# Optimization experiments

Hardware: AMD Instinct MI355X
Metric: run time of the kernel (lower is better)

The kernel has to match this reference:

```python
import jax, jax.numpy as jnp
import numpy as np
import math

H = 16          # num_heads
BS = 512        # block_size


def setup_inputs() -> dict:
    key = jax.random.key(0)
    ks = jax.random.split(key, 5)
    B, S, D = 2, 8192, 1024
    return {
        "x": jax.random.normal(ks[0], (B, S, D), dtype=jnp.float32),
        "W_qkv": jax.random.normal(ks[1], (D, 3 * D), dtype=jnp.float32) * (1.0 / math.sqrt(D)),
        "b_qkv": jax.random.normal(ks[2], (3 * D,), dtype=jnp.float32) * 0.02,
        "W_out": jax.random.normal(ks[3], (D, D), dtype=jnp.float32) * (1.0 / math.sqrt(D)),
        "b_out": jax.random.normal(ks[4], (D,), dtype=jnp.float32) * 0.02,
    }


def reference(x, W_qkv, b_qkv, W_out, b_out):
    B, S, D = x.shape
    hd = D // H
    nb = S // BS  # S chosen divisible by block_size, so no padding branch
    scale = 1.0 / math.sqrt(hd)

    qkv = (x @ W_qkv + b_qkv).reshape(B, S, 3, H, hd)
    qkv = jnp.transpose(qkv, (2, 0, 3, 1, 4))  # [3, B, H, S, hd]
    q, k, v = qkv[0], qkv[1], qkv[2]

    # split into blocks: [B, H, nb, BS, hd]
    qb = q.reshape(B, H, nb, BS, hd)
    kb = k.reshape(B, H, nb, BS, hd)
    vb = v.reshape(B, H, nb, BS, hd)

    # local block attention (separate softmax, as in original)
    s1 = jnp.einsum('bhnid,bhnjd->bhnij', qb, kb) * scale
    o1 = jnp.einsum('bhnij,bhnjd->bhnid', jax.nn.softmax(s1, axis=-1), vb)

    # next-block (ring) attention with its own softmax, then summed
    kn = jnp.roll(kb, -1, axis=2)
    vn = jnp.roll(vb, -1, axis=2)
    s2 = jnp.einsum('bhnid,bhnjd->bhnij', qb, kn) * scale
    o2 = jnp.einsum('bhnij,bhnjd->bhnid', jax.nn.softmax(s2, axis=-1), vn)

    out = (o1 + o2).reshape(B, H, S, hd)            # [B, H, S, hd]
    out = jnp.transpose(out, (0, 2, 1, 3)).reshape(B, S, D)
    return out @ W_out + b_out
```

## Files before the change

kernel.cpp:

```cpp
#include <hip/hip_runtime.h>
#include <hip/hip_bf16.h>

typedef __attribute__((ext_vector_type(4))) float f32x4;
typedef __attribute__((ext_vector_type(8))) short s16x8;
typedef __attribute__((address_space(3))) unsigned int lds_uint;
typedef __attribute__((address_space(1))) const unsigned int g_uint;

static __device__ __forceinline__ unsigned short f2b(float f) {
    union { __hip_bfloat16 h; unsigned short u; } c;
    c.h = __float2bfloat16(f);
    return c.u;
}

static __device__ __forceinline__ void async_copy16(const void* gsrc, void* ldst) {
    __builtin_amdgcn_global_load_lds((g_uint*)gsrc, (lds_uint*)ldst, 16, 0, 0);
}

__global__ __launch_bounds__(256) void cvt_x_kernel(const float* __restrict__ x,
                                                    unsigned short* __restrict__ xb) {
    long i = ((long)blockIdx.x * 256 + threadIdx.x) * 8;
    float4 a = *(const float4*)(x + i);
    float4 b = *(const float4*)(x + i + 4);
    union { unsigned short s[8]; s16x8 v; } o;
    o.s[0] = f2b(a.x); o.s[1] = f2b(a.y); o.s[2] = f2b(a.z); o.s[3] = f2b(a.w);
    o.s[4] = f2b(b.x); o.s[5] = f2b(b.y); o.s[6] = f2b(b.z); o.s[7] = f2b(b.w);
    *(s16x8*)(xb + i) = o.v;
}

__global__ __launch_bounds__(256) void cvt_wT_kernel(const float* __restrict__ W,
                                                     unsigned short* __restrict__ Wt,
                                                     int K, int N) {
    __shared__ float T[64][65];
    int nbk = K >> 6;
    int bk = blockIdx.x % nbk;
    int bn = blockIdx.x / nbk;
    int t = threadIdx.x;
    int r = t >> 4, c4 = (t & 15) << 2;
#pragma unroll
    for (int rd = 0; rd < 4; ++rd) {
        int row = rd * 16 + r;
        float4 v = *(const float4*)(W + (long)(bk * 64 + row) * N + bn * 64 + c4);
        T[row][c4 + 0] = v.x; T[row][c4 + 1] = v.y;
        T[row][c4 + 2] = v.z; T[row][c4 + 3] = v.w;
    }
    __syncthreads();
#pragma unroll
    for (int rd = 0; rd < 4; ++rd) {
        int nrow = rd * 16 + r;
        union { unsigned short s[4]; unsigned long long u; } o;
#pragma unroll
        for (int j = 0; j < 4; ++j) o.s[j] = f2b(T[c4 + j][nrow]);
        *(unsigned long long*)(Wt + (long)(bn * 64 + nrow) * K + bk * 64 + c4) = o.u;
    }
}

template<int OM>
__global__ __launch_bounds__(512) void gemm256_kernel(const unsigned short* __restrict__ A,
                                                      const unsigned short* __restrict__ Bt,
                                                      const float* __restrict__ bias,
                                                      unsigned short* __restrict__ qkb,
                                                      unsigned short* __restrict__ vT,
                                                      float* __restrict__ Cf,
                                                      int ntileN) {
    __shared__ char lds[131072];
    const int tid = threadIdx.x;
    const int w = tid >> 6, wm = w >> 2, wn = w & 3;
    const int l = tid & 63, c = l & 15, g = l >> 4;
    const int cpx = gridDim.x >> 3;
    const int wg = (blockIdx.x & 7) * cpx + (blockIdx.x >> 3);
    const int tm = wg / ntileN, tn = wg % ntileN;
    const long m0 = (long)tm << 8, n0 = (long)tn << 8;
    const int swg = (g ^ ((c >> 1) & 3)) << 4;
    const int ssch = (tid & 3) ^ ((tid >> 3) & 3);
    const int rb = tid >> 2;

    f32x4 acc[8][4];
#pragma unroll
    for (int i = 0; i < 8; ++i)
#pragma unroll
        for (int j = 0; j < 4; ++j) acc[i][j] = (f32x4){0.f, 0.f, 0.f, 0.f};

#define STG(panel, p0, u, kh, isB) do { \
    char* blk_ = lds + ((isB) ? 65536 : 0) + (((((u) & 1) * 2 + (kh))) << 14); \
    const unsigned short* sp_ = (panel) + (u) * 64 + (kh) * 32 + ssch * 8; \
    async_copy16(sp_ + ((p0) + rb) * 1024L, blk_ + tid * 16); \
    async_copy16(sp_ + ((p0) + 128 + rb) * 1024L, blk_ + 8192 + tid * 16); \
} while (0)

    STG(Bt, n0, 0, 0, 1); STG(A, m0, 0, 0, 0); STG(Bt, n0, 0, 1, 1); STG(A, m0, 0, 1, 0);
    STG(Bt, n0, 1, 0, 1); STG(A, m0, 1, 0, 0); STG(Bt, n0, 1, 1, 1);
    asm volatile("s_waitcnt vmcnt(10)");
    __builtin_amdgcn_s_barrier();
    __builtin_amdgcn_sched_barrier(0);

#define PHASE_MFMA(IBASE) \
    __builtin_amdgcn_s_setprio(1); \
    _Pragma("unroll") for (int i_ = 0; i_ < 4; ++i_) \
    _Pragma("unroll") for (int j_ = 0; j_ < 4; ++j_) \
        acc[(IBASE) + i_][j_] = __builtin_amdgcn_mfma_f32_16x16x32_bf16(af[i_], bf[j_], acc[(IBASE) + i_][j_], 0, 0, 0); \
    __builtin_amdgcn_s_setprio(0);

#define GSTEP(s, ST1, ST2, ST3, ST4, VMID, VEND) do { \
    const int buf_ = (s) & 1; \
    const char* LA0 = lds + ((buf_ * 2 + 0) << 14); \
    const char* LA1 = lds + ((buf_ * 2 + 1) << 14); \
    const char* LB0 = lds + 65536 + ((buf_ * 2 + 0) << 14); \
    const char* LB1 = lds + 65536 + ((buf_ * 2 + 1) << 14); \
    s16x8 af[4], bf[4]; \
    _Pragma("unroll") for (int i = 0; i < 4; ++i) af[i] = *(const s16x8*)(LA0 + (wm * 128 + i * 16 + c) * 64 + swg); \
    _Pragma("unroll") for (int j = 0; j < 4; ++j) bf[j] = *(const s16x8*)(LB0 + (wn * 64 + j * 16 + c) * 64 + swg); \
    if (ST1) STG(A, m0, (s) + 1, 1, 0); \
    __builtin_amdgcn_s_barrier(); \
    PHASE_MFMA(0) \
    __builtin_amdgcn_s_barrier(); \
    __builtin_amdgcn_sched_barrier(0); \
    _Pragma("unroll") for (int i = 0; i < 4; ++i) af[i] = *(const s16x8*)(LA0 + (wm * 128 + (4 + i) * 16 + c) * 64 + swg); \
    if (ST2) STG(Bt, n0, (s) + 2, 0, 1); \
    __builtin_amdgcn_s_barrier(); \
    PHASE_MFMA(4) \
    asm volatile("s_waitcnt " VMID); \
    __builtin_amdgcn_s_barrier(); \
    __builtin_amdgcn_sched_barrier(0); \
    _Pragma("unroll") for (int i = 0; i < 4; ++i) af[i] = *(const s16x8*)(LA1 + (wm * 128 + i * 16 + c) * 64 + swg); \
    _Pragma("unroll") for (int j = 0; j < 4; ++j) bf[j] = *(const s16x8*)(LB1 + (wn * 64 + j * 16 + c) * 64 + swg); \
    if (ST3) STG(A, m0, (s) + 2, 0, 0); \
    __builtin_amdgcn_s_barrier(); \
    PHASE_MFMA(0) \
    __builtin_amdgcn_s_barrier(); \
    __builtin_amdgcn_sched_barrier(0); \
    _Pragma("unroll") for (int i = 0; i < 4; ++i) af[i] = *(const s16x8*)(LA1 + (wm * 128 + (4 + i) * 16 + c) * 64 + swg); \
    if (ST4) STG(Bt, n0, (s) + 2, 1, 1); \
    __builtin_amdgcn_s_barrier(); \
    PHASE_MFMA(4) \
    if (VEND) { asm volatile("s_waitcnt " VMID##_E); } \
    __builtin_amdgcn_s_barrier(); \
    __builtin_amdgcn_sched_barrier(0); \
} while (0)

#define VM10 "vmcnt(10)"
#define VM10_E "vmcnt(10)"
#define VM8 "vmcnt(8)"
#define VM8_E "vmcnt(4)"
#define VM0 "vmcnt(0)"
#define VM0_E "vmcnt(0)"

    for (int s = 0; s < 14; ++s) GSTEP(s, 1, 1, 1, 1, VM10, 1);
    GSTEP(14, 1, 0, 0, 0, VM8, 1);
    GSTEP(15, 0, 0, 0, 0, VM0, 0);

    const long mrow0 = m0 + wm * 128;
    const int ncol0 = (int)n0 + wn * 64;
    if (OM == 0) {
        if (ncol0 < 2048) {
#pragma unroll
            for (int j = 0; j < 4; ++j) {
                int n = ncol0 + j * 16 + c;
                float bv = bias[n];
#pragma unroll
                for (int i = 0; i < 8; ++i)
#pragma unroll
                    for (int r = 0; r < 4; ++r) {
                        long m = mrow0 + i * 16 + 4 * g + r;
                        qkb[m * 2048 + n] = f2b(acc[i][j][r] + bv);
                    }
            }
        } else {
#pragma unroll
            for (int j = 0; j < 4; ++j) {
                int n = ncol0 + j * 16 + c;
                float bv = bias[n];
                int h = (n - 2048) >> 6, hd = n & 63;
#pragma unroll
                for (int i = 0; i < 8; ++i) {
                    long m = mrow0 + i * 16 + 4 * g;
                    long bb = m >> 13, ss = m & 8191;
                    union { unsigned short sh[4]; unsigned long long u; } o;
#pragma unroll
                    for (int r = 0; r < 4; ++r) o.sh[r] = f2b(acc[i][j][r] + bv);
                    *(unsigned long long*)(vT + ((bb * 16 + h) * 64 + hd) * 8192 + ss) = o.u;
                }
            }
        }
    } else {
#pragma unroll
        for (int j = 0; j < 4; ++j) {
            int n = ncol0 + j * 16 + c;
            float bv = bias[n];
#pragma unroll
            for (int i = 0; i < 8; ++i)
#pragma unroll
                for (int r = 0; r < 4; ++r) {
                    long m = mrow0 + i * 16 + 4 * g + r;
                    Cf[m * 1024 + n] = acc[i][j][r] + bv;
                }
        }
    }
#undef STG
#undef PHASE_MFMA
#undef GSTEP
}

__global__ __launch_bounds__(256) void attn_kernel(const unsigned short* __restrict__ qkb,
                                                   const unsigned short* __restrict__ vT,
                                                   unsigned short* __restrict__ outp) {
    __shared__ __align__(16) char KV[4][8192];
    __shared__ unsigned short Pws[4][32 * 72];
    const int bid = blockIdx.x;
    const int wgid = (bid & 7) * 256 + (bid >> 3);
    const int qt = wgid & 3;
    const int nblk = (wgid >> 2) & 15;
    const int h = (wgid >> 6) & 15;
    const int b = wgid >> 10;
    const int tid = threadIdx.x;
    const int w = tid >> 6, l = tid & 63;
    const int c = l & 15, g = l >> 4;

    const long qrow0 = (long)b * 8192 + nblk * 512 + qt * 128 + w * 32 + c;
    s16x8 qf[2][2];
#pragma unroll
    for (int qg = 0; qg < 2; ++qg) {
        const unsigned short* qp = qkb + (qrow0 + qg * 16) * 2048 + h * 64;
        qf[qg][0] = *(const s16x8*)(qp + g * 8);
        qf[qg][1] = *(const s16x8*)(qp + 32 + g * 8);
    }

    char* pw = (char*)(&Pws[w][0]);
    const float C2 = 0.125f * 1.44269504088896f;

    const int cl = tid & 7, rw = tid >> 3;
    const int sc = cl ^ (rw & 7);
    const int kb1 = (nblk + 1) & 15;
    const unsigned short* Kg0 = qkb + ((long)b * 8192 + nblk * 512 + rw) * 2048 + 1024 + h * 64 + sc * 8;
    const unsigned short* Kg1 = qkb + ((long)b * 8192 + kb1 * 512 + rw) * 2048 + 1024 + h * 64 + sc * 8;
    const unsigned short* Vg0 = vT + ((long)(b * 16 + h) * 64 + rw) * 8192 + nblk * 512 + sc * 8;
    const unsigned short* Vg1 = vT + ((long)(b * 16 + h) * 64 + rw) * 8192 + kb1 * 512 + sc * 8;

#define STAGE(tile) do { \
    const unsigned short* kn_ = (((tile) & 8) ? Kg1 : Kg0) + ((long)((tile) & 7) << 17); \
    const unsigned short* vn_ = (((tile) & 8) ? Vg1 : Vg0) + (((tile) & 7) << 6); \
    char* kd_ = KV[(tile) & 1] + tid * 16; \
    char* vd_ = KV[2 + ((tile) & 1)] + tid * 16; \
    async_copy16(kn_, kd_); \
    async_copy16(kn_ + 32L * 2048, kd_ + 4096); \
    async_copy16(vn_, vd_); \
    async_copy16(vn_ + 32L * 8192, vd_ + 4096); \
} while (0)

    float outv[2][16];
#pragma unroll
    for (int qg = 0; qg < 2; ++qg)
#pragma unroll
        for (int i = 0; i < 16; ++i) outv[qg][i] = 0.f;
    f32x4 oac[2][4];
#pragma unroll
    for (int qg = 0; qg < 2; ++qg)
#pragma unroll
        for (int i = 0; i < 4; ++i) oac[qg][i] = (f32x4){0.f, 0.f, 0.f, 0.f};
    float mrun[2] = {-3e38f, -3e38f}, lrun[2] = {0.f, 0.f};

    const int ch0 = (g ^ (c & 7)) << 4;

    STAGE(0);

    for (int it = 0; it < 16; ++it) {
        if (it < 15) {
            STAGE(it + 1);
            asm volatile("s_waitcnt vmcnt(4)" ::: "memory");
        } else {
            asm volatile("s_waitcnt vmcnt(0)" ::: "memory");
        }
        __builtin_amdgcn_s_barrier();
        __builtin_amdgcn_sched_barrier(0);

        const char* Kc = KV[it & 1];
        const char* Vc = KV[2 + (it & 1)];

        f32x4 sac[2][4];
#pragma unroll
        for (int qg = 0; qg < 2; ++qg)
#pragma unroll
            for (int i = 0; i < 4; ++i) sac[qg][i] = (f32x4){0.f, 0.f, 0.f, 0.f};
        __builtin_amdgcn_s_setprio(1);
#pragma unroll
        for (int kt = 0; kt < 4; ++kt) {
            const char* kr = Kc + (kt * 16 + c) * 128;
            s16x8 a0 = *(const s16x8*)(kr + ch0);
            s16x8 a1 = *(const s16x8*)(kr + (ch0 ^ 64));
            sac[0][kt] = __builtin_amdgcn_mfma_f32_16x16x32_bf16(a0, qf[0][0], sac[0][kt], 0, 0, 0);
            sac[0][kt] = __builtin_amdgcn_mfma_f32_16x16x32_bf16(a1, qf[0][1], sac[0][kt], 0, 0, 0);
            sac[1][kt] = __builtin_amdgcn_mfma_f32_16x16x32_bf16(a0, qf[1][0], sac[1][kt], 0, 0, 0);
            sac[1][kt] = __builtin_amdgcn_mfma_f32_16x16x32_bf16(a1, qf[1][1], sac[1][kt], 0, 0, 0);
        }
        __builtin_amdgcn_s_setprio(0);

#pragma unroll
        for (int qg = 0; qg < 2; ++qg) {
            float mx = sac[qg][0][0];
#pragma unroll
            for (int kt = 0; kt < 4; ++kt)
#pragma unroll
                for (int r = 0; r < 4; ++r) mx = fmaxf(mx, sac[qg][kt][r]);
            mx = fmaxf(mx, __shfl_xor(mx, 16, 64));
            mx = fmaxf(mx, __shfl_xor(mx, 32, 64));
            float mnew = fmaxf(mrun[qg], mx);
            float alpha = exp2f((mrun[qg] - mnew) * C2);
            float ls = 0.f;
#pragma unroll
            for (int kt = 0; kt < 4; ++kt) {
                union { unsigned short sh[4]; unsigned long long u; } pk;
#pragma unroll
                for (int r = 0; r < 4; ++r) {
                    float e = exp2f((sac[qg][kt][r] - mnew) * C2);
                    ls += e;
                    pk.sh[r] = f2b(e);
                }
                *(unsigned long long*)(pw + (qg * 16 + c) * 144 + kt * 32 + g * 8) = pk.u;
            }
            lrun[qg] = lrun[qg] * alpha + ls;
            mrun[qg] = mnew;
#pragma unroll
            for (int i = 0; i < 4; ++i) oac[qg][i] *= alpha;
        }

        __builtin_amdgcn_s_setprio(1);
#pragma unroll
        for (int kf = 0; kf < 2; ++kf) {
            s16x8 pf0 = *(const s16x8*)(pw + c * 144 + kf * 64 + g * 16);
            s16x8 pf1 = *(const s16x8*)(pw + (16 + c) * 144 + kf * 64 + g * 16);
#pragma unroll
            for (int ht = 0; ht < 4; ++ht) {
                s16x8 vf = *(const s16x8*)(Vc + (ht * 16 + c) * 128 + (ch0 ^ (kf << 6)));
                oac[0][ht] = __builtin_amdgcn_mfma_f32_16x16x32_bf16(vf, pf0, oac[0][ht], 0, 0, 0);
                oac[1][ht] = __builtin_amdgcn_mfma_f32_16x16x32_bf16(vf, pf1, oac[1][ht], 0, 0, 0);
            }
        }
        __builtin_amdgcn_s_setprio(0);

        if ((it & 7) == 7) {
#pragma unroll
            for (int qg = 0; qg < 2; ++qg) {
                float lt = lrun[qg];
                lt += __shfl_xor(lt, 16, 64);
                lt += __shfl_xor(lt, 32, 64);
                float inv = 1.f / lt;
#pragma unroll
                for (int i = 0; i < 16; ++i) outv[qg][i] += oac[qg][i >> 2][i & 3] * inv;
#pragma unroll
                for (int i = 0; i < 4; ++i) oac[qg][i] = (f32x4){0.f, 0.f, 0.f, 0.f};
                mrun[qg] = -3e38f;
                lrun[qg] = 0.f;
            }
        }
        __builtin_amdgcn_sched_barrier(0);
        __builtin_amdgcn_s_barrier();
        __builtin_amdgcn_sched_barrier(0);
    }
#undef STAGE

#pragma unroll
    for (int qg = 0; qg < 2; ++qg) {
        unsigned short* op = outp + (qrow0 + qg * 16) * 1024 + h * 64;
#pragma unroll
        for (int ht = 0; ht < 4; ++ht) {
            union { unsigned short sh[4]; unsigned long long u; } o;
#pragma unroll
            for (int r = 0; r < 4; ++r) o.sh[r] = f2b(outv[qg][ht * 4 + r]);
            *(unsigned long long*)(op + ht * 16 + 4 * g) = o.u;
        }
    }
}

extern "C" void kernel_launch(void* const* d_in, const int* in_sizes, int n_in,
                              void* d_out, int out_size, void* d_ws, size_t ws_size,
                              hipStream_t stream) {
    const float* x    = (const float*)d_in[0];
    const float* Wqkv = (const float*)d_in[1];
    const float* bqkv = (const float*)d_in[2];
    const float* Wout = (const float*)d_in[3];
    const float* bout = (const float*)d_in[4];
    float* out = (float*)d_out;

    char* ws = (char*)d_ws;
    unsigned short* xbf   = (unsigned short*)ws;
    unsigned short* wqkvT = (unsigned short*)(ws + 33554432);
    unsigned short* woutT = (unsigned short*)(ws + 39845888);
    unsigned short* qkb   = (unsigned short*)(ws + 41943040);
    unsigned short* vT    = (unsigned short*)(ws + 109051904);
    unsigned short* attn  = xbf;

    cvt_x_kernel<<<8192, 256, 0, stream>>>(x, xbf);
    cvt_wT_kernel<<<(1024 / 64) * (3072 / 64), 256, 0, stream>>>(Wqkv, wqkvT, 1024, 3072);
    cvt_wT_kernel<<<(1024 / 64) * (1024 / 64), 256, 0, stream>>>(Wout, woutT, 1024, 1024);
    gemm256_kernel<0><<<64 * 12, 512, 0, stream>>>(xbf, wqkvT, bqkv, qkb, vT, nullptr, 12);
    attn_kernel<<<2048, 256, 0, stream>>>(qkb, vT, attn);
    gemm256_kernel<1><<<64 * 4, 512, 0, stream>>>(attn, woutT, bout, nullptr, nullptr, out, 4);
}
```

Before: 431.9 us.

## Lazy softmax rescale, per-query-group P buffer with XOR swizzle, occupancy hint

The online-softmax rescale of the running max, sum and output accumulators now runs only when some lane's new max exceeds the stored max by more than a threshold (8 in log2 units), so most iterations skip the alpha exp and the accumulator multiplies. The P tile staging buffer shrinks to one 16-row slice per query group, using an XOR swizzle in place of padding, and the PV MFMAs for each group run right after that group's softmax. Launch bounds now request 4 blocks per SM. Risks are extra register pressure from the occupancy hint, serialization between P write and read for each group, and bf16 P values up to 256 in the lazy-rescale path.

```diff
diff --git a/kernel.cpp b/kernel.cpp
--- a/kernel.cpp
+++ b/kernel.cpp
@@ -200,11 +200,11 @@
 #undef GSTEP
 }
 
-__global__ __launch_bounds__(256) void attn_kernel(const unsigned short* __restrict__ qkb,
-                                                   const unsigned short* __restrict__ vT,
-                                                   unsigned short* __restrict__ outp) {
+__global__ __launch_bounds__(256, 4) void attn_kernel(const unsigned short* __restrict__ qkb,
+                                                      const unsigned short* __restrict__ vT,
+                                                      unsigned short* __restrict__ outp) {
     __shared__ __align__(16) char KV[4][8192];
-    __shared__ unsigned short Pws[4][32 * 72];
+    __shared__ __align__(16) char Pb[4][2048];
     const int bid = blockIdx.x;
     const int wgid = (bid & 7) * 256 + (bid >> 3);
     const int qt = wgid & 3;
@@ -224,7 +224,8 @@
         qf[qg][1] = *(const s16x8*)(qp + 32 + g * 8);
     }
 
-    char* pw = (char*)(&Pws[w][0]);
+    char* pw = Pb[w];
+    const int psw = (c & 7) << 4;
     const float C2 = 0.125f * 1.44269504088896f;
 
     const int cl = tid & 7, rw = tid >> 3;
@@ -295,46 +296,48 @@
 
 #pragma unroll
         for (int qg = 0; qg < 2; ++qg) {
-            float mx = sac[qg][0][0];
-#pragma unroll
-            for (int kt = 0; kt < 4; ++kt)
-#pragma unroll
-                for (int r = 0; r < 4; ++r) mx = fmaxf(mx, sac[qg][kt][r]);
+            float t0 = fmaxf(fmaxf(sac[qg][0][0], sac[qg][0][1]), fmaxf(sac[qg][0][2], sac[qg][0][3]));
+            float t1 = fmaxf(fmaxf(sac[qg][1][0], sac[qg][1][1]), fmaxf(sac[qg][1][2], sac[qg][1][3]));
+            float t2 = fmaxf(fmaxf(sac[qg][2][0], sac[qg][2][1]), fmaxf(sac[qg][2][2], sac[qg][2][3]));
+            float t3 = fmaxf(fmaxf(sac[qg][3][0], sac[qg][3][1]), fmaxf(sac[qg][3][2], sac[qg][3][3]));
+            float mx = fmaxf(fmaxf(t0, t1), fmaxf(t2, t3));
             mx = fmaxf(mx, __shfl_xor(mx, 16, 64));
             mx = fmaxf(mx, __shfl_xor(mx, 32, 64));
-            float mnew = fmaxf(mrun[qg], mx);
-            float alpha = exp2f((mrun[qg] - mnew) * C2);
+            if (!__all((mx - mrun[qg]) * C2 <= 8.0f)) {
+                float mnew = fmaxf(mrun[qg], mx);
+                float alpha = exp2f((mrun[qg] - mnew) * C2);
+                lrun[qg] *= alpha;
+#pragma unroll
+                for (int i = 0; i < 4; ++i) oac[qg][i] *= alpha;
+                mrun[qg] = mnew;
+            }
+            const float m = mrun[qg];
             float ls = 0.f;
 #pragma unroll
             for (int kt = 0; kt < 4; ++kt) {
                 union { unsigned short sh[4]; unsigned long long u; } pk;
 #pragma unroll
                 for (int r = 0; r < 4; ++r) {
-                    float e = exp2f((sac[qg][kt][r] - mnew) * C2);
+                    float e = exp2f((sac[qg][kt][r] - m) * C2);
                     ls += e;
                     pk.sh[r] = f2b(e);
                 }
-                *(unsigned long long*)(pw + (qg * 16 + c) * 144 + kt * 32 + g * 8) = pk.u;
-            }
-            lrun[qg] = lrun[qg] * alpha + ls;
-            mrun[qg] = mnew;
-#pragma unroll
-            for (int i = 0; i < 4; ++i) oac[qg][i] *= alpha;
-        }
-
-        __builtin_amdgcn_s_setprio(1);
-#pragma unroll
-        for (int kf = 0; kf < 2; ++kf) {
-            s16x8 pf0 = *(const s16x8*)(pw + c * 144 + kf * 64 + g * 16);
-            s16x8 pf1 = *(const s16x8*)(pw + (16 + c) * 144 + kf * 64 + g * 16);
-#pragma unroll
-            for (int ht = 0; ht < 4; ++ht) {
-                s16x8 vf = *(const s16x8*)(Vc + (ht * 16 + c) * 128 + (ch0 ^ (kf << 6)));
-                oac[0][ht] = __builtin_amdgcn_mfma_f32_16x16x32_bf16(vf, pf0, oac[0][ht], 0, 0, 0);
-                oac[1][ht] = __builtin_amdgcn_mfma_f32_16x16x32_bf16(vf, pf1, oac[1][ht], 0, 0, 0);
-            }
-        }
-        __builtin_amdgcn_s_setprio(0);
+                *(unsigned long long*)(pw + c * 128 + ((kt * 32 + g * 8) ^ psw)) = pk.u;
+            }
+            lrun[qg] += ls;
+
+            __builtin_amdgcn_s_setprio(1);
+#pragma unroll
+            for (int kf = 0; kf < 2; ++kf) {
+                s16x8 pf = *(const s16x8*)(pw + c * 128 + ((kf * 64 + g * 16) ^ psw));
+#pragma unroll
+                for (int ht = 0; ht < 4; ++ht) {
+                    s16x8 vf = *(const s16x8*)(Vc + (ht * 16 + c) * 128 + (ch0 ^ (kf << 6)));
+                    oac[qg][ht] = __builtin_amdgcn_mfma_f32_16x16x32_bf16(vf, pf, oac[qg][ht], 0, 0, 0);
+                }
+            }
+            __builtin_amdgcn_s_setprio(0);
+        }
 
         if ((it & 7) == 7) {
 #pragma unroll
```

Measured after the change: 444.8 us. 3.0% more time.
